# Kernel optimization log

Hardware: AMD Instinct MI355X
Metric: run time of the kernel (lower is better)

The kernel has to match this reference:

```python
import jax, jax.numpy as jnp
import numpy as np

N, E, H, IN_FEAT, NUM_GRAPHS, NUM_CLASSES, L, HID = 50000, 600000, 128, 7, 256, 2, 5, 256
EPS_MSG = 1e-7
EPS_SOFTMAX = 1e-16
LN_EPS = 1e-5


def layer_norm(x, g, b):
    mu = jnp.mean(x, axis=-1, keepdims=True)
    var = jnp.mean((x - mu) ** 2, axis=-1, keepdims=True)
    return (x - mu) * jax.lax.rsqrt(var + LN_EPS) * g + b


def setup_inputs() -> dict:
    key = jax.random.key(0)
    ks = jax.random.split(key, 16)
    s = 0.05
    return {
        "x": jax.random.normal(ks[0], (N, IN_FEAT), jnp.float32),
        "edge_index": jax.random.randint(ks[1], (2, E), 0, N),
        "batch": jnp.sort(jax.random.randint(ks[2], (N,), 0, NUM_GRAPHS)),
        "enc_W": jax.random.normal(ks[3], (IN_FEAT, H), jnp.float32) * s,
        "enc_b": jnp.zeros((H,), jnp.float32),
        "t": jnp.ones((L,), jnp.float32),  # learn_t, init t=1.0
        "W1": jax.random.normal(ks[4], (L, H, HID), jnp.float32) * s,
        "b1": jnp.zeros((L, HID), jnp.float32),
        "g1": jnp.ones((L, HID), jnp.float32),
        "bb1": jnp.zeros((L, HID), jnp.float32),
        "W2": jax.random.normal(ks[5], (L, HID, H), jnp.float32) * s,
        "b2": jnp.zeros((L, H), jnp.float32),
        "ln_g": jnp.ones((L, H), jnp.float32),
        "ln_b": jnp.zeros((L, H), jnp.float32),
        "cls_W": jax.random.normal(ks[6], (H, NUM_CLASSES), jnp.float32) * s,
        "cls_b": jnp.zeros((NUM_CLASSES,), jnp.float32),
    }


def reference(x, edge_index, batch, enc_W, enc_b, t, W1, b1, g1, bb1, W2, b2, ln_g, ln_b, cls_W, cls_b):
    n = x.shape[0]
    src, dst = edge_index[0], edge_index[1]  # messages flow src -> dst
    h = x @ enc_W + enc_b  # node_encoder, [N, H]
    for i in range(t.shape[0]):  # DeepGCNLayer, block='res+'
        z = jax.nn.relu(layer_norm(h, ln_g[i], ln_b[i]))
        # GENConv message: relu(x_j) + eps (edge_attr is None)
        msg = jax.nn.relu(z[src]) + EPS_MSG  # [E, H]
        # scatter-softmax aggregation with temperature t
        logits = msg * t[i]
        m = jax.ops.segment_max(logits, dst, num_segments=n)  # [N, H]
        ex = jnp.exp(logits - m[dst])
        den = jax.ops.segment_sum(ex, dst, num_segments=n) + EPS_SOFTMAX
        agg = jax.ops.segment_sum(ex * msg, dst, num_segments=n) / den
        # GENConv update MLP: Linear -> LayerNorm -> ReLU -> Linear on (agg + x)
        out = agg + z
        hm = jax.nn.relu(layer_norm(out @ W1[i] + b1[i], g1[i], bb1[i]))
        h = h + (hm @ W2[i] + b2[i])  # residual
    pooled = jax.ops.segment_sum(h, batch, num_segments=NUM_GRAPHS)  # global_add_pool
    return pooled @ cls_W + cls_b
```

## Files before the change

### kernel.cpp

```cpp
#include <hip/hip_runtime.h>
#include <hip/hip_bf16.h>

#define HD 128
#define HIDD 256
#define EPS_MSG 1e-7f
#define EPS_SM 1e-16f
#define LN_EPS 1e-5f
#define HP2 264
#define OBS 68
#define LOG2E 1.44269504f

typedef __attribute__((ext_vector_type(8))) short bf16x8;
typedef __attribute__((ext_vector_type(4))) float f32x4;
typedef __attribute__((ext_vector_type(4))) ushort u16x4;

static __device__ __forceinline__ float wave_reduce_sum(float v) {
#pragma unroll
    for (int off = 32; off >= 1; off >>= 1) v += __shfl_xor(v, off, 64);
    return v;
}

static __device__ __forceinline__ float u2f(unsigned v) {
    union { float f; unsigned u; } x;
    x.u = v;
    return x.f;
}
static __device__ __forceinline__ ushort f2bf(float f) {
    __hip_bfloat16 b = __float2bfloat16(f);
    return *(ushort*)&b;
}
static __device__ __forceinline__ unsigned packbf(float lo, float hi) {
    return (unsigned)f2bf(lo) | ((unsigned)f2bf(hi) << 16);
}

__global__ __launch_bounds__(256) void enc_ln_kernel(const float* __restrict__ x,
                                                     const float* __restrict__ W,
                                                     const float* __restrict__ b,
                                                     const float* __restrict__ g,
                                                     const float* __restrict__ bt,
                                                     unsigned* __restrict__ hp,
                                                     unsigned* __restrict__ zp, int N) {
    int node = blockIdx.x * 4 + (threadIdx.x >> 6);
    int lane = threadIdx.x & 63;
    if (node >= N) return;
    float xr[7];
#pragma unroll
    for (int j = 0; j < 7; ++j) xr[j] = x[node * 7 + j];
    float v0 = b[lane], v1 = b[lane + 64];
#pragma unroll
    for (int j = 0; j < 7; ++j) {
        v0 = fmaf(xr[j], W[j * HD + lane], v0);
        v1 = fmaf(xr[j], W[j * HD + lane + 64], v1);
    }
    float s = wave_reduce_sum(v0 + v1);
    float ss = wave_reduce_sum(v0 * v0 + v1 * v1);
    float mu = s * (1.f / 128.f);
    float var = ss * (1.f / 128.f) - mu * mu;
    float rstd = rsqrtf(var + LN_EPS);
    float z0 = fmaxf((v0 - mu) * rstd * g[lane] + bt[lane], 0.f);
    float z1 = fmaxf((v1 - mu) * rstd * g[lane + 64] + bt[lane + 64], 0.f);
    int i0 = (2 * lane) & 63, i1 = (2 * lane + 1) & 63;
    float he_lo = __shfl(v0, i0), ho_lo = __shfl(v0, i1);
    float he_hi = __shfl(v1, i0), ho_hi = __shfl(v1, i1);
    float hce = (lane < 32) ? he_lo : he_hi;
    float hco = (lane < 32) ? ho_lo : ho_hi;
    hp[(size_t)node * 64 + lane] = packbf(hce, hco);
    float e_lo = __shfl(z0, i0), o_lo = __shfl(z0, i1);
    float e_hi = __shfl(z1, i0), o_hi = __shfl(z1, i1);
    float ce = (lane < 32) ? e_lo : e_hi;
    float co = (lane < 32) ? o_lo : o_hi;
    zp[(size_t)node * 64 + lane] = packbf(ce, co);
}

__global__ __launch_bounds__(256) void wconv_kernel(const float* __restrict__ W1,
                                                    const float* __restrict__ W2,
                                                    ushort* __restrict__ W1t,
                                                    ushort* __restrict__ W2t, int L) {
    int gid = blockIdx.x * 256 + threadIdx.x;
    int per = HD * HIDD;
    int tot = L * per;
    if (gid < tot) {
        int l = gid / per, r = gid % per;
        int n = r >> 7, k = r & 127;
        W1t[gid] = f2bf(W1[(size_t)l * per + (size_t)k * HIDD + n]);
    } else if (gid < 2 * tot) {
        int g2 = gid - tot;
        int l = g2 / per, r = g2 % per;
        int n = r >> 8, k = r & 255;
        W2t[g2] = f2bf(W2[(size_t)l * per + (size_t)k * HD + n]);
    }
}

__global__ __launch_bounds__(256) void count_kernel(const int* __restrict__ dst, int* __restrict__ cnt, int E) {
    int e = blockIdx.x * 256 + threadIdx.x;
    if (e < E) atomicAdd(&cnt[dst[e]], 1);
}

__global__ __launch_bounds__(256) void scanA_kernel(const int* __restrict__ cnt, int* __restrict__ row_ptr,
                                                    int* __restrict__ blk_sums, int n) {
    __shared__ int sb[256];
    int tid = threadIdx.x;
    int idx = blockIdx.x * 256 + tid;
    int v = (idx < n) ? cnt[idx] : 0;
    sb[tid] = v;
    __syncthreads();
#pragma unroll
    for (int off = 1; off < 256; off <<= 1) {
        int x = (tid >= off) ? sb[tid - off] : 0;
        __syncthreads();
        sb[tid] += x;
        __syncthreads();
    }
    if (idx < n) row_ptr[idx + 1] = sb[tid];
    if (tid == 255) blk_sums[blockIdx.x] = sb[255];
}

__global__ __launch_bounds__(256) void scanB_kernel(int* __restrict__ blk_sums, int nblk) {
    __shared__ int sb[256];
    int tid = threadIdx.x;
    int v = (tid < nblk) ? blk_sums[tid] : 0;
    sb[tid] = v;
    __syncthreads();
#pragma unroll
    for (int off = 1; off < 256; off <<= 1) {
        int x = (tid >= off) ? sb[tid - off] : 0;
        __syncthreads();
        sb[tid] += x;
        __syncthreads();
    }
    if (tid < nblk) blk_sums[tid] = sb[tid];
}

__global__ __launch_bounds__(256) void scanC_kernel(int* __restrict__ row_ptr, const int* __restrict__ blk_sums, int n) {
    int idx = blockIdx.x * 256 + threadIdx.x;
    if (idx == 0) row_ptr[0] = 0;
    if (idx < n) {
        int b = idx >> 8;
        if (b > 0) row_ptr[idx + 1] += blk_sums[b - 1];
    }
}

__global__ __launch_bounds__(256) void cursor_init_kernel(const int* __restrict__ row_ptr, int* __restrict__ cursor, int n) {
    int idx = blockIdx.x * 256 + threadIdx.x;
    if (idx < n) cursor[idx] = row_ptr[idx];
}

__global__ __launch_bounds__(256) void scatter_kernel(const int* __restrict__ src, const int* __restrict__ dst,
                                                      int* __restrict__ cursor, int* __restrict__ esrc, int E) {
    int e = blockIdx.x * 256 + threadIdx.x;
    if (e < E) {
        int v = dst[e];
        int pos = atomicAdd(&cursor[v], 1);
        esrc[pos] = src[e];
    }
}

__global__ __launch_bounds__(256, 4) void layer_kernel(const unsigned* __restrict__ zp_in,
                                                       unsigned* __restrict__ zp_out,
                                                       unsigned* __restrict__ hp,
                                                       const int* __restrict__ row_ptr,
                                                       const int* __restrict__ esrc,
                                                       const float* __restrict__ t_all, int layer,
                                                       const ushort* __restrict__ W1t, const float* __restrict__ b1,
                                                       const float* __restrict__ g1, const float* __restrict__ bb1,
                                                       const ushort* __restrict__ W2t, const float* __restrict__ b2,
                                                       const float* __restrict__ gnext, const float* __restrict__ btnext,
                                                       int fuse, int N) {
    __shared__ unsigned s_ob[32 * OBS];
    __shared__ ushort s_hm[32 * HP2];
    __shared__ float s_part[32 * 8];

    int tid = threadIdx.x;
    int wid = tid >> 6, lane = tid & 63;
    int l15 = lane & 15, q = lane >> 4;
    int row0 = blockIdx.x * 32;

    uint2 hpre[2][2];
#pragma unroll
    for (int mb = 0; mb < 2; ++mb) {
        int row = row0 + mb * 16 + l15;
#pragma unroll
        for (int nb = 0; nb < 2; ++nb) {
            if (row < N)
                hpre[mb][nb] = *(const uint2*)&hp[(size_t)row * 64 + wid * 16 + nb * 8 + q * 2];
            else {
                hpre[mb][nb].x = 0u;
                hpre[mb][nb].y = 0u;
            }
        }
    }

    {
        const float tv = t_all[layer];
        const float M = 12.f * fmaxf(tv, 1.f);
        const float tv2 = tv * LOG2E;
        const float mM2 = -M * LOG2E;

#define AGG_EDGE(P, E0, E1, W0, W1)                                   \
    {                                                                  \
        float a0 = u2f((P) << 16) + EPS_MSG;                           \
        float a1 = u2f((P) & 0xffff0000u) + EPS_MSG;                   \
        float x0 = __builtin_amdgcn_exp2f(fmaf(a0, tv2, mM2));         \
        float x1 = __builtin_amdgcn_exp2f(fmaf(a1, tv2, mM2));         \
        E0 += x0;                                                      \
        E1 += x1;                                                      \
        W0 = fmaf(x0, a0, W0);                                         \
        W1 = fmaf(x1, a1, W1);                                         \
    }

        for (int j = 0; j < 8; ++j) {
            int nd = row0 + wid * 8 + j;
            if (nd >= N) break;
            int beg = __builtin_amdgcn_readfirstlane(row_ptr[nd]);
            int end = __builtin_amdgcn_readfirstlane(row_ptr[nd + 1]);
            float se0 = 0.f, se1 = 0.f, sw0 = 0.f, sw1 = 0.f;
            float te0 = 0.f, te1 = 0.f, tw0 = 0.f, tw1 = 0.f;
            int e = beg;
            for (; e + 4 <= end; e += 4) {
                int s0 = esrc[e], s1 = esrc[e + 1], s2 = esrc[e + 2], s3 = esrc[e + 3];
                unsigned p0 = zp_in[(size_t)s0 * 64 + lane];
                unsigned p1 = zp_in[(size_t)s1 * 64 + lane];
                unsigned p2 = zp_in[(size_t)s2 * 64 + lane];
                unsigned p3 = zp_in[(size_t)s3 * 64 + lane];
                AGG_EDGE(p0, se0, se1, sw0, sw1)
                AGG_EDGE(p1, se0, se1, sw0, sw1)
                AGG_EDGE(p2, te0, te1, tw0, tw1)
                AGG_EDGE(p3, te0, te1, tw0, tw1)
            }
            for (; e < end; ++e) {
                unsigned p0 = zp_in[(size_t)esrc[e] * 64 + lane];
                AGG_EDGE(p0, se0, se1, sw0, sw1)
            }
            se0 += te0; se1 += te1; sw0 += tw0; sw1 += tw1;
            float a0 = (end > beg) ? sw0 / (se0 + EPS_SM) : 0.f;
            float a1 = (end > beg) ? sw1 / (se1 + EPS_SM) : 0.f;
            unsigned ps = zp_in[(size_t)nd * 64 + lane];
            float z0 = u2f(ps << 16), z1 = u2f(ps & 0xffff0000u);
            s_ob[(wid * 8 + j) * OBS + lane] = packbf(a0 + z0, a1 + z1);
        }
#undef AGG_EDGE
    }
    __syncthreads();

    f32x4 acc1[2][4];
#pragma unroll
    for (int mb = 0; mb < 2; ++mb)
#pragma unroll
        for (int nb = 0; nb < 4; ++nb) acc1[mb][nb] = (f32x4)0.f;

#pragma unroll
    for (int kk = 0; kk < 4; ++kk) {
        bf16x8 bfr[2];
#pragma unroll
        for (int mb = 0; mb < 2; ++mb)
            bfr[mb] = *(const bf16x8*)&s_ob[(mb * 16 + l15) * OBS + kk * 16 + q * 4];
#pragma unroll
        for (int nb = 0; nb < 4; ++nb) {
            bf16x8 wfr = *(const bf16x8*)&W1t[(size_t)(wid * 64 + nb * 16 + l15) * HD + kk * 32 + q * 8];
#pragma unroll
            for (int mb = 0; mb < 2; ++mb)
                acc1[mb][nb] = __builtin_amdgcn_mfma_f32_16x16x32_bf16(wfr, bfr[mb], acc1[mb][nb], 0, 0, 0);
        }
    }

    f32x4 b1v[4];
#pragma unroll
    for (int nb = 0; nb < 4; ++nb) b1v[nb] = *(const f32x4*)&b1[wid * 64 + nb * 16 + q * 4];

#pragma unroll
    for (int mb = 0; mb < 2; ++mb) {
        float s = 0.f, ss = 0.f;
#pragma unroll
        for (int nb = 0; nb < 4; ++nb) {
#pragma unroll
            for (int rg = 0; rg < 4; ++rg) {
                float v = acc1[mb][nb][rg] + b1v[nb][rg];
                acc1[mb][nb][rg] = v;
                s += v;
                ss += v * v;
            }
        }
        s += __shfl_xor(s, 16, 64);
        s += __shfl_xor(s, 32, 64);
        ss += __shfl_xor(ss, 16, 64);
        ss += __shfl_xor(ss, 32, 64);
        if (q == 0) {
            s_part[(mb * 16 + l15) * 8 + wid * 2] = s;
            s_part[(mb * 16 + l15) * 8 + wid * 2 + 1] = ss;
        }
    }
    __syncthreads();

    f32x4 g1v[4], bbv[4];
#pragma unroll
    for (int nb = 0; nb < 4; ++nb) {
        g1v[nb] = *(const f32x4*)&g1[wid * 64 + nb * 16 + q * 4];
        bbv[nb] = *(const f32x4*)&bb1[wid * 64 + nb * 16 + q * 4];
    }
#pragma unroll
    for (int mb = 0; mb < 2; ++mb) {
        int rl = mb * 16 + l15;
        f32x4 p0 = *(const f32x4*)&s_part[rl * 8];
        f32x4 p1 = *(const f32x4*)&s_part[rl * 8 + 4];
        float S = p0.x + p0.z + p1.x + p1.z;
        float SS = p0.y + p0.w + p1.y + p1.w;
        float mu = S * (1.f / 256.f);
        float var = SS * (1.f / 256.f) - mu * mu;
        float rstd = rsqrtf(var + LN_EPS);
#pragma unroll
        for (int nb = 0; nb < 4; ++nb) {
            u16x4 pk;
#pragma unroll
            for (int rg = 0; rg < 4; ++rg) {
                float v = fmaxf((acc1[mb][nb][rg] - mu) * rstd * g1v[nb][rg] + bbv[nb][rg], 0.f);
                pk[rg] = f2bf(v);
            }
            *(u16x4*)&s_hm[rl * HP2 + wid * 64 + nb * 16 + q * 4] = pk;
        }
    }
    __syncthreads();

    f32x4 acc2[2][2];
#pragma unroll
    for (int mb = 0; mb < 2; ++mb)
#pragma unroll
        for (int nb = 0; nb < 2; ++nb) acc2[mb][nb] = (f32x4)0.f;

#pragma unroll
    for (int kk = 0; kk < 8; ++kk) {
        bf16x8 hfr[2];
#pragma unroll
        for (int mb = 0; mb < 2; ++mb)
            hfr[mb] = *(const bf16x8*)&s_hm[(mb * 16 + l15) * HP2 + kk * 32 + q * 8];
#pragma unroll
        for (int nb = 0; nb < 2; ++nb) {
            bf16x8 wfr = *(const bf16x8*)&W2t[(size_t)(wid * 32 + nb * 16 + l15) * HIDD + kk * 32 + q * 8];
#pragma unroll
            for (int mb = 0; mb < 2; ++mb)
                acc2[mb][nb] = __builtin_amdgcn_mfma_f32_16x16x32_bf16(wfr, hfr[mb], acc2[mb][nb], 0, 0, 0);
        }
    }

    f32x4 b2v[2];
#pragma unroll
    for (int nb = 0; nb < 2; ++nb) b2v[nb] = *(const f32x4*)&b2[wid * 32 + nb * 16 + q * 4];

#pragma unroll
    for (int mb = 0; mb < 2; ++mb) {
        int row = row0 + mb * 16 + l15;
        float s2 = 0.f, ss2 = 0.f;
        if (row < N) {
#pragma unroll
            for (int nb = 0; nb < 2; ++nb) {
                uint2 hv = hpre[mb][nb];
                float h0 = u2f(hv.x << 16), h1 = u2f(hv.x & 0xffff0000u);
                float h2 = u2f(hv.y << 16), h3 = u2f(hv.y & 0xffff0000u);
                f32x4 v;
                v[0] = h0 + acc2[mb][nb][0] + b2v[nb][0];
                v[1] = h1 + acc2[mb][nb][1] + b2v[nb][1];
                v[2] = h2 + acc2[mb][nb][2] + b2v[nb][2];
                v[3] = h3 + acc2[mb][nb][3] + b2v[nb][3];
                s2 += v[0] + v[1] + v[2] + v[3];
                ss2 += v[0] * v[0] + v[1] * v[1] + v[2] * v[2] + v[3] * v[3];
                uint2 pk;
                pk.x = packbf(v[0], v[1]);
                pk.y = packbf(v[2], v[3]);
                *(uint2*)&hp[(size_t)row * 64 + wid * 16 + nb * 8 + q * 2] = pk;
                acc2[mb][nb] = v;
            }
        }
        if (fuse) {
            s2 += __shfl_xor(s2, 16, 64);
            s2 += __shfl_xor(s2, 32, 64);
            ss2 += __shfl_xor(ss2, 16, 64);
            ss2 += __shfl_xor(ss2, 32, 64);
            if (q == 0) {
                s_part[(mb * 16 + l15) * 8 + wid * 2] = s2;
                s_part[(mb * 16 + l15) * 8 + wid * 2 + 1] = ss2;
            }
        }
    }

    if (fuse) {
        __syncthreads();
        f32x4 gnv[2], bnv[2];
#pragma unroll
        for (int nb = 0; nb < 2; ++nb) {
            gnv[nb] = *(const f32x4*)&gnext[wid * 32 + nb * 16 + q * 4];
            bnv[nb] = *(const f32x4*)&btnext[wid * 32 + nb * 16 + q * 4];
        }
#pragma unroll
        for (int mb = 0; mb < 2; ++mb) {
            int rl = mb * 16 + l15;
            int row = row0 + rl;
            f32x4 p0 = *(const f32x4*)&s_part[rl * 8];
            f32x4 p1 = *(const f32x4*)&s_part[rl * 8 + 4];
            float S = p0.x + p0.z + p1.x + p1.z;
            float SS = p0.y + p0.w + p1.y + p1.w;
            float mu = S * (1.f / 128.f);
            float var = SS * (1.f / 128.f) - mu * mu;
            float rstd = rsqrtf(var + LN_EPS);
            if (row < N) {
#pragma unroll
                for (int nb = 0; nb < 2; ++nb) {
                    float z0 = fmaxf((acc2[mb][nb][0] - mu) * rstd * gnv[nb][0] + bnv[nb][0], 0.f);
                    float z1 = fmaxf((acc2[mb][nb][1] - mu) * rstd * gnv[nb][1] + bnv[nb][1], 0.f);
                    float z2 = fmaxf((acc2[mb][nb][2] - mu) * rstd * gnv[nb][2] + bnv[nb][2], 0.f);
                    float z3 = fmaxf((acc2[mb][nb][3] - mu) * rstd * gnv[nb][3] + bnv[nb][3], 0.f);
                    uint2 pk;
                    pk.x = packbf(z0, z1);
                    pk.y = packbf(z2, z3);
                    *(uint2*)&zp_out[(size_t)row * 64 + wid * 16 + nb * 8 + q * 2] = pk;
                }
            }
        }
    }
}

__global__ __launch_bounds__(256) void pool_kernel(const unsigned* __restrict__ hp,
                                                   const int* __restrict__ batch, int N,
                                                   float* __restrict__ pooled) {
    __shared__ int sb[2];
    __shared__ float red0[256], red1[256];
    int g = blockIdx.x;
    if (threadIdx.x == 0) {
        int lo = 0, hi = N;
        while (lo < hi) { int mid = (lo + hi) >> 1; if (batch[mid] < g) lo = mid + 1; else hi = mid; }
        sb[0] = lo;
        lo = 0; hi = N;
        int gq = g + 1;
        while (lo < hi) { int mid = (lo + hi) >> 1; if (batch[mid] < gq) lo = mid + 1; else hi = mid; }
        sb[1] = lo;
    }
    __syncthreads();
    int beg = sb[0], end = sb[1];
    int c = threadIdx.x & 63, str = threadIdx.x >> 6;
    float a0 = 0.f, a1 = 0.f;
    for (int r = beg + str; r < end; r += 4) {
        unsigned p = hp[(size_t)r * 64 + c];
        a0 += u2f(p << 16);
        a1 += u2f(p & 0xffff0000u);
    }
    red0[threadIdx.x] = a0;
    red1[threadIdx.x] = a1;
    __syncthreads();
    if (str == 0) {
        float s0 = red0[c] + red0[64 + c] + red0[128 + c] + red0[192 + c];
        float s1 = red1[c] + red1[64 + c] + red1[128 + c] + red1[192 + c];
        pooled[(size_t)g * HD + 2 * c] = s0;
        pooled[(size_t)g * HD + 2 * c + 1] = s1;
    }
}

__global__ __launch_bounds__(256) void cls_kernel(const float* __restrict__ pooled,
                                                  const float* __restrict__ W,
                                                  const float* __restrict__ b,
                                                  float* __restrict__ out, int G) {
    int gid = blockIdx.x * 256 + threadIdx.x;
    if (gid >= G * 2) return;
    int g = gid >> 1, cl = gid & 1;
    float acc = b[cl];
#pragma unroll 8
    for (int k = 0; k < HD; ++k) acc += pooled[g * HD + k] * W[k * 2 + cl];
    out[gid] = acc;
}

extern "C" void kernel_launch(void* const* d_in, const int* in_sizes, int n_in,
                              void* d_out, int out_size, void* d_ws, size_t ws_size,
                              hipStream_t stream) {
    const float* x     = (const float*)d_in[0];
    const int*   eidx  = (const int*)d_in[1];
    const int*   batch = (const int*)d_in[2];
    const float* enc_W = (const float*)d_in[3];
    const float* enc_b = (const float*)d_in[4];
    const float* t_all = (const float*)d_in[5];
    const float* W1    = (const float*)d_in[6];
    const float* b1    = (const float*)d_in[7];
    const float* g1    = (const float*)d_in[8];
    const float* bb1   = (const float*)d_in[9];
    const float* W2    = (const float*)d_in[10];
    const float* b2    = (const float*)d_in[11];
    const float* ln_g  = (const float*)d_in[12];
    const float* ln_b  = (const float*)d_in[13];
    const float* cls_W = (const float*)d_in[14];
    const float* cls_b = (const float*)d_in[15];
    float* out = (float*)d_out;

    const int N = in_sizes[0] / 7;
    const int E = in_sizes[1] / 2;
    const int L = in_sizes[5];
    const int G = out_size / 2;
    const int* src = eidx;
    const int* dst = eidx + E;

    char* p = (char*)d_ws;
    auto alloc = [&](size_t bytes) {
        char* q = p;
        p += (bytes + 255) & ~(size_t)255;
        return q;
    };
    unsigned* hp     = (unsigned*)alloc((size_t)N * 64 * 4);
    unsigned* zp0    = (unsigned*)alloc((size_t)N * 64 * 4);
    unsigned* zp1    = (unsigned*)alloc((size_t)N * 64 * 4);
    float*    pooled = (float*)alloc((size_t)G * HD * 4);
    int* cnt      = (int*)alloc((size_t)N * 4);
    int* row_ptr  = (int*)alloc((size_t)(N + 1) * 4);
    int* cursor   = (int*)alloc((size_t)N * 4);
    int* blk_sums = (int*)alloc(256 * 4);
    int* esrc     = (int*)alloc((size_t)E * 4);
    ushort* W1t   = (ushort*)alloc((size_t)L * HD * HIDD * 2);
    ushort* W2t   = (ushort*)alloc((size_t)L * HD * HIDD * 2);

    unsigned* zpbuf[2] = {zp0, zp1};

    const int nblkN = (N + 255) / 256;
    const int nblkE = (E + 255) / 256;

    enc_ln_kernel<<<(N + 3) / 4, 256, 0, stream>>>(x, enc_W, enc_b, ln_g, ln_b, hp, zp0, N);
    {
        int tot2 = 2 * L * HD * HIDD;
        wconv_kernel<<<(tot2 + 255) / 256, 256, 0, stream>>>(W1, W2, W1t, W2t, L);
    }

    hipMemsetAsync(cnt, 0, (size_t)N * 4, stream);
    count_kernel<<<nblkE, 256, 0, stream>>>(dst, cnt, E);
    scanA_kernel<<<nblkN, 256, 0, stream>>>(cnt, row_ptr, blk_sums, N);
    scanB_kernel<<<1, 256, 0, stream>>>(blk_sums, nblkN);
    scanC_kernel<<<nblkN, 256, 0, stream>>>(row_ptr, blk_sums, N);
    cursor_init_kernel<<<nblkN, 256, 0, stream>>>(row_ptr, cursor, N);
    scatter_kernel<<<nblkE, 256, 0, stream>>>(src, dst, cursor, esrc, E);

    for (int i = 0; i < L; ++i) {
        int fuse = (i + 1 < L) ? 1 : 0;
        const float* gn = ln_g + (size_t)(fuse ? i + 1 : i) * HD;
        const float* bn = ln_b + (size_t)(fuse ? i + 1 : i) * HD;
        layer_kernel<<<(N + 31) / 32, 256, 0, stream>>>(zpbuf[i & 1], zpbuf[(i + 1) & 1], hp,
                                                        row_ptr, esrc, t_all, i,
                                                        W1t + (size_t)i * HD * HIDD, b1 + (size_t)i * HIDD,
                                                        g1 + (size_t)i * HIDD, bb1 + (size_t)i * HIDD,
                                                        W2t + (size_t)i * HD * HIDD, b2 + (size_t)i * HD,
                                                        gn, bn, fuse, N);
    }

    pool_kernel<<<G, 256, 0, stream>>>(hp, batch, N, pooled);
    cls_kernel<<<(G * 2 + 255) / 256, 256, 0, stream>>>(pooled, cls_W, cls_b, out, G);
}
```

Baseline: 544.0 us.

## Warp-specialize layer kernel: producer waves gather while consumer waves run MLP

The layer kernel becomes a persistent kernel of 512 blocks with 512 threads. Four producer waves do the softmax edge aggregation for the next 32-row tile into a double-buffered shared tile, while four consumer waves run the two MFMA GEMMs and layer norms on the previous tile. The goal is to overlap the latency-bound gather with the matrix work. The cursor-init kernel is also folded into scanC, removing one launch. The price is a fixed grid that may limit occupancy, extra barriers per step, and a deferred next-layer-norm flush that adds complexity.

```diff
diff --git a/kernel.cpp b/kernel.cpp
--- a/kernel.cpp
+++ b/kernel.cpp
@@ -131,18 +131,16 @@
     if (tid < nblk) blk_sums[tid] = sb[tid];
 }
 
-__global__ __launch_bounds__(256) void scanC_kernel(int* __restrict__ row_ptr, const int* __restrict__ blk_sums, int n) {
+__global__ __launch_bounds__(256) void scanC_kernel(int* __restrict__ row_ptr, const int* __restrict__ blk_sums,
+                                                    int* __restrict__ cursor, int n) {
     int idx = blockIdx.x * 256 + threadIdx.x;
-    if (idx == 0) row_ptr[0] = 0;
+    if (idx == 0) { row_ptr[0] = 0; cursor[0] = 0; }
     if (idx < n) {
         int b = idx >> 8;
-        if (b > 0) row_ptr[idx + 1] += blk_sums[b - 1];
-    }
-}
-
-__global__ __launch_bounds__(256) void cursor_init_kernel(const int* __restrict__ row_ptr, int* __restrict__ cursor, int n) {
-    int idx = blockIdx.x * 256 + threadIdx.x;
-    if (idx < n) cursor[idx] = row_ptr[idx];
+        int v = row_ptr[idx + 1] + ((b > 0) ? blk_sums[b - 1] : 0);
+        row_ptr[idx + 1] = v;
+        if (idx + 1 < n) cursor[idx + 1] = v;
+    }
 }
 
 __global__ __launch_bounds__(256) void scatter_kernel(const int* __restrict__ src, const int* __restrict__ dst,
@@ -155,7 +153,7 @@
     }
 }
 
-__global__ __launch_bounds__(256, 4) void layer_kernel(const unsigned* __restrict__ zp_in,
+__global__ __launch_bounds__(512, 4) void layer_kernel(const unsigned* __restrict__ zp_in,
                                                        unsigned* __restrict__ zp_out,
                                                        unsigned* __restrict__ hp,
                                                        const int* __restrict__ row_ptr,
@@ -165,36 +163,31 @@
                                                        const float* __restrict__ g1, const float* __restrict__ bb1,
                                                        const ushort* __restrict__ W2t, const float* __restrict__ b2,
                                                        const float* __restrict__ gnext, const float* __restrict__ btnext,
-                                                       int fuse, int N) {
-    __shared__ unsigned s_ob[32 * OBS];
+                                                       int fuse, int ntiles, int N) {
+    __shared__ unsigned s_ob[2][32 * OBS];
     __shared__ ushort s_hm[32 * HP2];
     __shared__ float s_part[32 * 8];
-
-    int tid = threadIdx.x;
-    int wid = tid >> 6, lane = tid & 63;
-    int l15 = lane & 15, q = lane >> 4;
-    int row0 = blockIdx.x * 32;
-
+    __shared__ float s_part2[32 * 8];
+
+    const int tid = threadIdx.x;
+    const int wid = tid >> 6;
+    const int lane = tid & 63;
+    const int l15 = lane & 15, q = lane >> 4;
+    const bool isProd = wid < 4;
+    const int wc = wid & 3;
+
+    const float tv = t_all[layer];
+    const float Mc = 12.f * fmaxf(tv, 1.f);
+    const float tv2 = tv * LOG2E;
+    const float mM2 = -Mc * LOG2E;
+
+    const int myT = (ntiles > (int)blockIdx.x) ? ((ntiles - 1 - (int)blockIdx.x) / (int)gridDim.x + 1) : 0;
+
+    f32x4 acc1[2][4];
+    f32x4 acc2s[2][2];
     uint2 hpre[2][2];
-#pragma unroll
-    for (int mb = 0; mb < 2; ++mb) {
-        int row = row0 + mb * 16 + l15;
-#pragma unroll
-        for (int nb = 0; nb < 2; ++nb) {
-            if (row < N)
-                hpre[mb][nb] = *(const uint2*)&hp[(size_t)row * 64 + wid * 16 + nb * 8 + q * 2];
-            else {
-                hpre[mb][nb].x = 0u;
-                hpre[mb][nb].y = 0u;
-            }
-        }
-    }
-
-    {
-        const float tv = t_all[layer];
-        const float M = 12.f * fmaxf(tv, 1.f);
-        const float tv2 = tv * LOG2E;
-        const float mM2 = -M * LOG2E;
+    int prevRow0 = -1;
+    int row0 = 0;
 
 #define AGG_EDGE(P, E0, E1, W0, W1)                                   \
     {                                                                  \
@@ -208,213 +201,247 @@
         W1 = fmaf(x1, a1, W1);                                         \
     }
 
-        for (int j = 0; j < 8; ++j) {
-            int nd = row0 + wid * 8 + j;
-            if (nd >= N) break;
-            int beg = __builtin_amdgcn_readfirstlane(row_ptr[nd]);
-            int end = __builtin_amdgcn_readfirstlane(row_ptr[nd + 1]);
-            float se0 = 0.f, se1 = 0.f, sw0 = 0.f, sw1 = 0.f;
-            float te0 = 0.f, te1 = 0.f, tw0 = 0.f, tw1 = 0.f;
-            int e = beg;
-            for (; e + 4 <= end; e += 4) {
-                int s0 = esrc[e], s1 = esrc[e + 1], s2 = esrc[e + 2], s3 = esrc[e + 3];
-                unsigned p0 = zp_in[(size_t)s0 * 64 + lane];
-                unsigned p1 = zp_in[(size_t)s1 * 64 + lane];
-                unsigned p2 = zp_in[(size_t)s2 * 64 + lane];
-                unsigned p3 = zp_in[(size_t)s3 * 64 + lane];
-                AGG_EDGE(p0, se0, se1, sw0, sw1)
-                AGG_EDGE(p1, se0, se1, sw0, sw1)
-                AGG_EDGE(p2, te0, te1, tw0, tw1)
-                AGG_EDGE(p3, te0, te1, tw0, tw1)
-            }
-            for (; e < end; ++e) {
-                unsigned p0 = zp_in[(size_t)esrc[e] * 64 + lane];
-                AGG_EDGE(p0, se0, se1, sw0, sw1)
-            }
-            se0 += te0; se1 += te1; sw0 += tw0; sw1 += tw1;
-            float a0 = (end > beg) ? sw0 / (se0 + EPS_SM) : 0.f;
-            float a1 = (end > beg) ? sw1 / (se1 + EPS_SM) : 0.f;
-            unsigned ps = zp_in[(size_t)nd * 64 + lane];
-            float z0 = u2f(ps << 16), z1 = u2f(ps & 0xffff0000u);
-            s_ob[(wid * 8 + j) * OBS + lane] = packbf(a0 + z0, a1 + z1);
+#define PROD_CHUNK(J0, J1)                                                            \
+    {                                                                                  \
+        int gt32 = (blockIdx.x + step * gridDim.x) * 32;                               \
+        unsigned* ob = &s_ob[step & 1][0];                                             \
+        for (int j = (J0); j < (J1); ++j) {                                            \
+            int nd = gt32 + wc * 8 + j;                                                \
+            int lr = wc * 8 + j;                                                       \
+            if (nd < N) {                                                              \
+                int beg = __builtin_amdgcn_readfirstlane(row_ptr[nd]);                 \
+                int end = __builtin_amdgcn_readfirstlane(row_ptr[nd + 1]);             \
+                unsigned ps = zp_in[(size_t)nd * 64 + lane];                           \
+                float se0 = 0.f, se1 = 0.f, sw0 = 0.f, sw1 = 0.f;                      \
+                float te0 = 0.f, te1 = 0.f, tw0 = 0.f, tw1 = 0.f;                      \
+                int e = beg;                                                           \
+                for (; e + 4 <= end; e += 4) {                                         \
+                    int s0 = esrc[e], s1 = esrc[e + 1], s2 = esrc[e + 2], s3 = esrc[e + 3]; \
+                    unsigned p0 = zp_in[(size_t)s0 * 64 + lane];                       \
+                    unsigned p1 = zp_in[(size_t)s1 * 64 + lane];                       \
+                    unsigned p2 = zp_in[(size_t)s2 * 64 + lane];                       \
+                    unsigned p3 = zp_in[(size_t)s3 * 64 + lane];                       \
+                    AGG_EDGE(p0, se0, se1, sw0, sw1)                                   \
+                    AGG_EDGE(p1, se0, se1, sw0, sw1)                                   \
+                    AGG_EDGE(p2, te0, te1, tw0, tw1)                                   \
+                    AGG_EDGE(p3, te0, te1, tw0, tw1)                                   \
+                }                                                                      \
+                for (; e < end; ++e) {                                                 \
+                    unsigned p0 = zp_in[(size_t)esrc[e] * 64 + lane];                  \
+                    AGG_EDGE(p0, se0, se1, sw0, sw1)                                   \
+                }                                                                      \
+                se0 += te0; se1 += te1; sw0 += tw0; sw1 += tw1;                        \
+                float a0 = (end > beg) ? sw0 / (se0 + EPS_SM) : 0.f;                   \
+                float a1 = (end > beg) ? sw1 / (se1 + EPS_SM) : 0.f;                   \
+                float z0 = u2f(ps << 16), z1 = u2f(ps & 0xffff0000u);                  \
+                ob[lr * OBS + lane] = packbf(a0 + z0, a1 + z1);                        \
+            } else {                                                                   \
+                ob[lr * OBS + lane] = 0u;                                              \
+            }                                                                          \
+        }                                                                              \
+    }
+
+#define ZP_FLUSH                                                                       \
+    {                                                                                  \
+        f32x4 gnv[2], bnv[2];                                                          \
+        for (int nb = 0; nb < 2; ++nb) {                                               \
+            gnv[nb] = *(const f32x4*)&gnext[wc * 32 + nb * 16 + q * 4];                \
+            bnv[nb] = *(const f32x4*)&btnext[wc * 32 + nb * 16 + q * 4];               \
+        }                                                                              \
+        for (int mb = 0; mb < 2; ++mb) {                                               \
+            int rl = mb * 16 + l15;                                                    \
+            int row = prevRow0 + rl;                                                   \
+            f32x4 p0 = *(const f32x4*)&s_part2[rl * 8];                                \
+            f32x4 p1 = *(const f32x4*)&s_part2[rl * 8 + 4];                            \
+            float S = p0.x + p0.z + p1.x + p1.z;                                       \
+            float SS = p0.y + p0.w + p1.y + p1.w;                                      \
+            float mu = S * (1.f / 128.f);                                              \
+            float var = SS * (1.f / 128.f) - mu * mu;                                  \
+            float rstd = rsqrtf(var + LN_EPS);                                         \
+            if (row < N) {                                                             \
+                for (int nb = 0; nb < 2; ++nb) {                                       \
+                    float z0 = fmaxf((acc2s[mb][nb][0] - mu) * rstd * gnv[nb][0] + bnv[nb][0], 0.f); \
+                    float z1 = fmaxf((acc2s[mb][nb][1] - mu) * rstd * gnv[nb][1] + bnv[nb][1], 0.f); \
+                    float z2 = fmaxf((acc2s[mb][nb][2] - mu) * rstd * gnv[nb][2] + bnv[nb][2], 0.f); \
+                    float z3 = fmaxf((acc2s[mb][nb][3] - mu) * rstd * gnv[nb][3] + bnv[nb][3], 0.f); \
+                    uint2 pk;                                                          \
+                    pk.x = packbf(z0, z1);                                             \
+                    pk.y = packbf(z2, z3);                                             \
+                    *(uint2*)&zp_out[(size_t)row * 64 + wc * 16 + nb * 8 + q * 2] = pk; \
+                }                                                                      \
+            }                                                                          \
+        }                                                                              \
+    }
+
+    for (int step = 0; step <= myT; ++step) {
+        if (isProd) {
+            if (step < myT) PROD_CHUNK(0, 3)
+        } else if (step >= 1) {
+            row0 = (blockIdx.x + (step - 1) * gridDim.x) * 32;
+            if (fuse && prevRow0 >= 0) ZP_FLUSH
+#pragma unroll
+            for (int mb = 0; mb < 2; ++mb) {
+                int row = row0 + mb * 16 + l15;
+#pragma unroll
+                for (int nb = 0; nb < 2; ++nb) {
+                    if (row < N)
+                        hpre[mb][nb] = *(const uint2*)&hp[(size_t)row * 64 + wc * 16 + nb * 8 + q * 2];
+                    else {
+                        hpre[mb][nb].x = 0u;
+                        hpre[mb][nb].y = 0u;
+                    }
+                }
+            }
+            const unsigned* ob = &s_ob[(step - 1) & 1][0];
+#pragma unroll
+            for (int mb = 0; mb < 2; ++mb)
+#pragma unroll
+                for (int nb = 0; nb < 4; ++nb) acc1[mb][nb] = (f32x4)0.f;
+#pragma unroll
+            for (int kk = 0; kk < 4; ++kk) {
+                bf16x8 bfr[2];
+#pragma unroll
+                for (int mb = 0; mb < 2; ++mb)
+                    bfr[mb] = *(const bf16x8*)&ob[(mb * 16 + l15) * OBS + kk * 16 + q * 4];
+#pragma unroll
+                for (int nb = 0; nb < 4; ++nb) {
+                    bf16x8 wfr = *(const bf16x8*)&W1t[(size_t)(wc * 64 + nb * 16 + l15) * HD + kk * 32 + q * 8];
+#pragma unroll
+                    for (int mb = 0; mb < 2; ++mb)
+                        acc1[mb][nb] = __builtin_amdgcn_mfma_f32_16x16x32_bf16(wfr, bfr[mb], acc1[mb][nb], 0, 0, 0);
+                }
+            }
+            f32x4 b1v[4];
+#pragma unroll
+            for (int nb = 0; nb < 4; ++nb) b1v[nb] = *(const f32x4*)&b1[wc * 64 + nb * 16 + q * 4];
+#pragma unroll
+            for (int mb = 0; mb < 2; ++mb) {
+                float s = 0.f, ss = 0.f;
+#pragma unroll
+                for (int nb = 0; nb < 4; ++nb) {
+#pragma unroll
+                    for (int rg = 0; rg < 4; ++rg) {
+                        float v = acc1[mb][nb][rg] + b1v[nb][rg];
+                        acc1[mb][nb][rg] = v;
+                        s += v;
+                        ss += v * v;
+                    }
+                }
+                s += __shfl_xor(s, 16, 64);
+                s += __shfl_xor(s, 32, 64);
+                ss += __shfl_xor(ss, 16, 64);
+                ss += __shfl_xor(ss, 32, 64);
+                if (q == 0) {
+                    s_part[(mb * 16 + l15) * 8 + wc * 2] = s;
+                    s_part[(mb * 16 + l15) * 8 + wc * 2 + 1] = ss;
+                }
+            }
         }
+        __syncthreads();
+
+        if (isProd) {
+            if (step < myT) PROD_CHUNK(3, 6)
+        } else if (step >= 1) {
+            f32x4 g1v[4], bbv[4];
+#pragma unroll
+            for (int nb = 0; nb < 4; ++nb) {
+                g1v[nb] = *(const f32x4*)&g1[wc * 64 + nb * 16 + q * 4];
+                bbv[nb] = *(const f32x4*)&bb1[wc * 64 + nb * 16 + q * 4];
+            }
+#pragma unroll
+            for (int mb = 0; mb < 2; ++mb) {
+                int rl = mb * 16 + l15;
+                f32x4 p0 = *(const f32x4*)&s_part[rl * 8];
+                f32x4 p1 = *(const f32x4*)&s_part[rl * 8 + 4];
+                float S = p0.x + p0.z + p1.x + p1.z;
+                float SS = p0.y + p0.w + p1.y + p1.w;
+                float mu = S * (1.f / 256.f);
+                float var = SS * (1.f / 256.f) - mu * mu;
+                float rstd = rsqrtf(var + LN_EPS);
+#pragma unroll
+                for (int nb = 0; nb < 4; ++nb) {
+                    u16x4 pk;
+#pragma unroll
+                    for (int rg = 0; rg < 4; ++rg) {
+                        float v = fmaxf((acc1[mb][nb][rg] - mu) * rstd * g1v[nb][rg] + bbv[nb][rg], 0.f);
+                        pk[rg] = f2bf(v);
+                    }
+                    *(u16x4*)&s_hm[rl * HP2 + wc * 64 + nb * 16 + q * 4] = pk;
+                }
+            }
+        }
+        __syncthreads();
+
+        if (isProd) {
+            if (step < myT) PROD_CHUNK(6, 8)
+        } else if (step >= 1) {
+            f32x4 acc2[2][2];
+#pragma unroll
+            for (int mb = 0; mb < 2; ++mb)
+#pragma unroll
+                for (int nb = 0; nb < 2; ++nb) acc2[mb][nb] = (f32x4)0.f;
+#pragma unroll
+            for (int kk = 0; kk < 8; ++kk) {
+                bf16x8 hfr[2];
+#pragma unroll
+                for (int mb = 0; mb < 2; ++mb)
+                    hfr[mb] = *(const bf16x8*)&s_hm[(mb * 16 + l15) * HP2 + kk * 32 + q * 8];
+#pragma unroll
+                for (int nb = 0; nb < 2; ++nb) {
+                    bf16x8 wfr = *(const bf16x8*)&W2t[(size_t)(wc * 32 + nb * 16 + l15) * HIDD + kk * 32 + q * 8];
+#pragma unroll
+                    for (int mb = 0; mb < 2; ++mb)
+                        acc2[mb][nb] = __builtin_amdgcn_mfma_f32_16x16x32_bf16(wfr, hfr[mb], acc2[mb][nb], 0, 0, 0);
+                }
+            }
+            f32x4 b2v[2];
+#pragma unroll
+            for (int nb = 0; nb < 2; ++nb) b2v[nb] = *(const f32x4*)&b2[wc * 32 + nb * 16 + q * 4];
+#pragma unroll
+            for (int mb = 0; mb < 2; ++mb) {
+                int row = row0 + mb * 16 + l15;
+                float s2 = 0.f, ss2 = 0.f;
+                if (row < N) {
+#pragma unroll
+                    for (int nb = 0; nb < 2; ++nb) {
+                        uint2 hv = hpre[mb][nb];
+                        float h0 = u2f(hv.x << 16), h1 = u2f(hv.x & 0xffff0000u);
+                        float h2 = u2f(hv.y << 16), h3 = u2f(hv.y & 0xffff0000u);
+                        f32x4 v;
+                        v[0] = h0 + acc2[mb][nb][0] + b2v[nb][0];
+                        v[1] = h1 + acc2[mb][nb][1] + b2v[nb][1];
+                        v[2] = h2 + acc2[mb][nb][2] + b2v[nb][2];
+                        v[3] = h3 + acc2[mb][nb][3] + b2v[nb][3];
+                        s2 += v[0] + v[1] + v[2] + v[3];
+                        ss2 += v[0] * v[0] + v[1] * v[1] + v[2] * v[2] + v[3] * v[3];
+                        uint2 pk;
+                        pk.x = packbf(v[0], v[1]);
+                        pk.y = packbf(v[2], v[3]);
+                        *(uint2*)&hp[(size_t)row * 64 + wc * 16 + nb * 8 + q * 2] = pk;
+                        acc2s[mb][nb] = v;
+                    }
+                }
+                if (fuse) {
+                    s2 += __shfl_xor(s2, 16, 64);
+                    s2 += __shfl_xor(s2, 32, 64);
+                    ss2 += __shfl_xor(ss2, 16, 64);
+                    ss2 += __shfl_xor(ss2, 32, 64);
+                    if (q == 0) {
+                        s_part2[(mb * 16 + l15) * 8 + wc * 2] = s2;
+                        s_part2[(mb * 16 + l15) * 8 + wc * 2 + 1] = ss2;
+                    }
+                }
+            }
+            prevRow0 = row0;
+        }
+        __syncthreads();
+    }
+
+    if (!isProd && fuse && prevRow0 >= 0) ZP_FLUSH
+
 #undef AGG_EDGE
-    }
-    __syncthreads();
-
-    f32x4 acc1[2][4];
-#pragma unroll
-    for (int mb = 0; mb < 2; ++mb)
-#pragma unroll
-        for (int nb = 0; nb < 4; ++nb) acc1[mb][nb] = (f32x4)0.f;
-
-#pragma unroll
-    for (int kk = 0; kk < 4; ++kk) {
-        bf16x8 bfr[2];
-#pragma unroll
-        for (int mb = 0; mb < 2; ++mb)
-            bfr[mb] = *(const bf16x8*)&s_ob[(mb * 16 + l15) * OBS + kk * 16 + q * 4];
-#pragma unroll
-        for (int nb = 0; nb < 4; ++nb) {
-            bf16x8 wfr = *(const bf16x8*)&W1t[(size_t)(wid * 64 + nb * 16 + l15) * HD + kk * 32 + q * 8];
-#pragma unroll
-            for (int mb = 0; mb < 2; ++mb)
-                acc1[mb][nb] = __builtin_amdgcn_mfma_f32_16x16x32_bf16(wfr, bfr[mb], acc1[mb][nb], 0, 0, 0);
-        }
-    }
-
-    f32x4 b1v[4];
-#pragma unroll
-    for (int nb = 0; nb < 4; ++nb) b1v[nb] = *(const f32x4*)&b1[wid * 64 + nb * 16 + q * 4];
-
-#pragma unroll
-    for (int mb = 0; mb < 2; ++mb) {
-        float s = 0.f, ss = 0.f;
-#pragma unroll
-        for (int nb = 0; nb < 4; ++nb) {
-#pragma unroll
-            for (int rg = 0; rg < 4; ++rg) {
-                float v = acc1[mb][nb][rg] + b1v[nb][rg];
-                acc1[mb][nb][rg] = v;
-                s += v;
-                ss += v * v;
-            }
-        }
-        s += __shfl_xor(s, 16, 64);
-        s += __shfl_xor(s, 32, 64);
-        ss += __shfl_xor(ss, 16, 64);
-        ss += __shfl_xor(ss, 32, 64);
-        if (q == 0) {
-            s_part[(mb * 16 + l15) * 8 + wid * 2] = s;
-            s_part[(mb * 16 + l15) * 8 + wid * 2 + 1] = ss;
-        }
-    }
-    __syncthreads();
-
-    f32x4 g1v[4], bbv[4];
-#pragma unroll
-    for (int nb = 0; nb < 4; ++nb) {
-        g1v[nb] = *(const f32x4*)&g1[wid * 64 + nb * 16 + q * 4];
-        bbv[nb] = *(const f32x4*)&bb1[wid * 64 + nb * 16 + q * 4];
-    }
-#pragma unroll
-    for (int mb = 0; mb < 2; ++mb) {
-        int rl = mb * 16 + l15;
-        f32x4 p0 = *(const f32x4*)&s_part[rl * 8];
-        f32x4 p1 = *(const f32x4*)&s_part[rl * 8 + 4];
-        float S = p0.x + p0.z + p1.x + p1.z;
-        float SS = p0.y + p0.w + p1.y + p1.w;
-        float mu = S * (1.f / 256.f);
-        float var = SS * (1.f / 256.f) - mu * mu;
-        float rstd = rsqrtf(var + LN_EPS);
-#pragma unroll
-        for (int nb = 0; nb < 4; ++nb) {
-            u16x4 pk;
-#pragma unroll
-            for (int rg = 0; rg < 4; ++rg) {
-                float v = fmaxf((acc1[mb][nb][rg] - mu) * rstd * g1v[nb][rg] + bbv[nb][rg], 0.f);
-                pk[rg] = f2bf(v);
-            }
-            *(u16x4*)&s_hm[rl * HP2 + wid * 64 + nb * 16 + q * 4] = pk;
-        }
-    }
-    __syncthreads();
-
-    f32x4 acc2[2][2];
-#pragma unroll
-    for (int mb = 0; mb < 2; ++mb)
-#pragma unroll
-        for (int nb = 0; nb < 2; ++nb) acc2[mb][nb] = (f32x4)0.f;
-
-#pragma unroll
-    for (int kk = 0; kk < 8; ++kk) {
-        bf16x8 hfr[2];
-#pragma unroll
-        for (int mb = 0; mb < 2; ++mb)
-            hfr[mb] = *(const bf16x8*)&s_hm[(mb * 16 + l15) * HP2 + kk * 32 + q * 8];
-#pragma unroll
-        for (int nb = 0; nb < 2; ++nb) {
-            bf16x8 wfr = *(const bf16x8*)&W2t[(size_t)(wid * 32 + nb * 16 + l15) * HIDD + kk * 32 + q * 8];
-#pragma unroll
-            for (int mb = 0; mb < 2; ++mb)
-                acc2[mb][nb] = __builtin_amdgcn_mfma_f32_16x16x32_bf16(wfr, hfr[mb], acc2[mb][nb], 0, 0, 0);
-        }
-    }
-
-    f32x4 b2v[2];
-#pragma unroll
-    for (int nb = 0; nb < 2; ++nb) b2v[nb] = *(const f32x4*)&b2[wid * 32 + nb * 16 + q * 4];
-
-#pragma unroll
-    for (int mb = 0; mb < 2; ++mb) {
-        int row = row0 + mb * 16 + l15;
-        float s2 = 0.f, ss2 = 0.f;
-        if (row < N) {
-#pragma unroll
-            for (int nb = 0; nb < 2; ++nb) {
-                uint2 hv = hpre[mb][nb];
-                float h0 = u2f(hv.x << 16), h1 = u2f(hv.x & 0xffff0000u);
-                float h2 = u2f(hv.y << 16), h3 = u2f(hv.y & 0xffff0000u);
-                f32x4 v;
-                v[0] = h0 + acc2[mb][nb][0] + b2v[nb][0];
-                v[1] = h1 + acc2[mb][nb][1] + b2v[nb][1];
-                v[2] = h2 + acc2[mb][nb][2] + b2v[nb][2];
-                v[3] = h3 + acc2[mb][nb][3] + b2v[nb][3];
-                s2 += v[0] + v[1] + v[2] + v[3];
-                ss2 += v[0] * v[0] + v[1] * v[1] + v[2] * v[2] + v[3] * v[3];
-                uint2 pk;
-                pk.x = packbf(v[0], v[1]);
-                pk.y = packbf(v[2], v[3]);
-                *(uint2*)&hp[(size_t)row * 64 + wid * 16 + nb * 8 + q * 2] = pk;
-                acc2[mb][nb] = v;
-            }
-        }
-        if (fuse) {
-            s2 += __shfl_xor(s2, 16, 64);
-            s2 += __shfl_xor(s2, 32, 64);
-            ss2 += __shfl_xor(ss2, 16, 64);
-            ss2 += __shfl_xor(ss2, 32, 64);
-            if (q == 0) {
-                s_part[(mb * 16 + l15) * 8 + wid * 2] = s2;
-                s_part[(mb * 16 + l15) * 8 + wid * 2 + 1] = ss2;
-            }
-        }
-    }
-
-    if (fuse) {
-        __syncthreads();
-        f32x4 gnv[2], bnv[2];
-#pragma unroll
-        for (int nb = 0; nb < 2; ++nb) {
-            gnv[nb] = *(const f32x4*)&gnext[wid * 32 + nb * 16 + q * 4];
-            bnv[nb] = *(const f32x4*)&btnext[wid * 32 + nb * 16 + q * 4];
-        }
-#pragma unroll
-        for (int mb = 0; mb < 2; ++mb) {
-            int rl = mb * 16 + l15;
-            int row = row0 + rl;
-            f32x4 p0 = *(const f32x4*)&s_part[rl * 8];
-            f32x4 p1 = *(const f32x4*)&s_part[rl * 8 + 4];
-            float S = p0.x + p0.z + p1.x + p1.z;
-            float SS = p0.y + p0.w + p1.y + p1.w;
-            float mu = S * (1.f / 128.f);
-            float var = SS * (1.f / 128.f) - mu * mu;
-            float rstd = rsqrtf(var + LN_EPS);
-            if (row < N) {
-#pragma unroll
-                for (int nb = 0; nb < 2; ++nb) {
-                    float z0 = fmaxf((acc2[mb][nb][0] - mu) * rstd * gnv[nb][0] + bnv[nb][0], 0.f);
-                    float z1 = fmaxf((acc2[mb][nb][1] - mu) * rstd * gnv[nb][1] + bnv[nb][1], 0.f);
-                    float z2 = fmaxf((acc2[mb][nb][2] - mu) * rstd * gnv[nb][2] + bnv[nb][2], 0.f);
-                    float z3 = fmaxf((acc2[mb][nb][3] - mu) * rstd * gnv[nb][3] + bnv[nb][3], 0.f);
-                    uint2 pk;
-                    pk.x = packbf(z0, z1);
-                    pk.y = packbf(z2, z3);
-                    *(uint2*)&zp_out[(size_t)row * 64 + wid * 16 + nb * 8 + q * 2] = pk;
-                }
-            }
-        }
-    }
+#undef PROD_CHUNK
+#undef ZP_FLUSH
 }
 
 __global__ __launch_bounds__(256) void pool_kernel(const unsigned* __restrict__ hp,
@@ -515,6 +542,7 @@
 
     const int nblkN = (N + 255) / 256;
     const int nblkE = (E + 255) / 256;
+    const int ntiles = (N + 31) / 32;
 
     enc_ln_kernel<<<(N + 3) / 4, 256, 0, stream>>>(x, enc_W, enc_b, ln_g, ln_b, hp, zp0, N);
     {
@@ -526,20 +554,19 @@
     count_kernel<<<nblkE, 256, 0, stream>>>(dst, cnt, E);
     scanA_kernel<<<nblkN, 256, 0, stream>>>(cnt, row_ptr, blk_sums, N);
     scanB_kernel<<<1, 256, 0, stream>>>(blk_sums, nblkN);
-    scanC_kernel<<<nblkN, 256, 0, stream>>>(row_ptr, blk_sums, N);
-    cursor_init_kernel<<<nblkN, 256, 0, stream>>>(row_ptr, cursor, N);
+    scanC_kernel<<<nblkN, 256, 0, stream>>>(row_ptr, blk_sums, cursor, N);
     scatter_kernel<<<nblkE, 256, 0, stream>>>(src, dst, cursor, esrc, E);
 
     for (int i = 0; i < L; ++i) {
         int fuse = (i + 1 < L) ? 1 : 0;
         const float* gn = ln_g + (size_t)(fuse ? i + 1 : i) * HD;
         const float* bn = ln_b + (size_t)(fuse ? i + 1 : i) * HD;
-        layer_kernel<<<(N + 31) / 32, 256, 0, stream>>>(zpbuf[i & 1], zpbuf[(i + 1) & 1], hp,
-                                                        row_ptr, esrc, t_all, i,
-                                                        W1t + (size_t)i * HD * HIDD, b1 + (size_t)i * HIDD,
-                                                        g1 + (size_t)i * HIDD, bb1 + (size_t)i * HIDD,
-                                                        W2t + (size_t)i * HD * HIDD, b2 + (size_t)i * HD,
-                                                        gn, bn, fuse, N);
+        layer_kernel<<<512, 512, 0, stream>>>(zpbuf[i & 1], zpbuf[(i + 1) & 1], hp,
+                                              row_ptr, esrc, t_all, i,
+                                              W1t + (size_t)i * HD * HIDD, b1 + (size_t)i * HIDD,
+                                              g1 + (size_t)i * HIDD, bb1 + (size_t)i * HIDD,
+                                              W2t + (size_t)i * HD * HIDD, b2 + (size_t)i * HD,
+                                              gn, bn, fuse, ntiles, N);
     }
 
     pool_kernel<<<G, 256, 0, stream>>>(hp, batch, N, pooled);
```

Result: slower. 754.8 us (+38.7%).
